# Optimization experiments

Measured on AMD Instinct MI355X. Metric: run time of the kernel, lower is better.

The kernel has to match this reference:

```python
import jax, jax.numpy as jnp
import numpy as np

N_NODES = 50000
N_EDGES = 800000
IN_DIM, HID_DIM, OUT_DIM = 64, 128, 128


def _glorot(key, shape):
    fan_in, fan_out = shape[1], shape[0]
    lim = float(np.sqrt(6.0 / (fan_in + fan_out)))
    return jax.random.uniform(key, shape, jnp.float32, -lim, lim)


def setup_inputs() -> dict:
    key = jax.random.key(0)
    ks = jax.random.split(key, 8)
    x = jax.random.normal(ks[0], (N_NODES, IN_DIM), jnp.float32)
    edge_index = jax.random.randint(ks[1], (2, N_EDGES), 0, N_NODES, jnp.int64)
    return {
        "x": x,
        "edge_index": edge_index,
        # layer 1 (SAGEConv: lin_l acts on aggregated neighbors + bias, lin_r on root)
        "W1_l": _glorot(ks[2], (HID_DIM, IN_DIM)),
        "W1_r": _glorot(ks[3], (HID_DIM, IN_DIM)),
        "b1": jnp.zeros((HID_DIM,), jnp.float32),
        # layer 2
        "W2_l": _glorot(ks[4], (OUT_DIM, HID_DIM)),
        "W2_r": _glorot(ks[5], (OUT_DIM, HID_DIM)),
        "b2": jnp.zeros((OUT_DIM,), jnp.float32),
    }


def _sage_conv(x, src, dst, W_l, W_r, b):
    # mean aggregation of neighbor features: messages flow src -> dst
    msg = x[src]                                           # [E, D]
    agg = jax.ops.segment_sum(msg, dst, num_segments=N_NODES)  # [N, D]
    deg = jax.ops.segment_sum(jnp.ones((msg.shape[0],), x.dtype), dst,
                              num_segments=N_NODES)        # [N]
    mean = agg / jnp.maximum(deg, 1.0)[:, None]            # isolated nodes -> 0
    return mean @ W_l.T + x @ W_r.T + b


def reference(x, edge_index, W1_l, W1_r, b1, W2_l, W2_r, b2):
    src, dst = edge_index[0], edge_index[1]
    h = _sage_conv(x, src, dst, W1_l, W1_r, b1)
    h = jax.nn.relu(h)
    out = _sage_conv(h, src, dst, W2_l, W2_r, b2)
    return out
```

## Files before the change

### kernel.cpp

```cpp
#include <hip/hip_runtime.h>
#include <hip/hip_bf16.h>

constexpr int N  = 50000;
constexpr int E  = 800000;
constexpr int D0 = 64;
constexpr int D1 = 128;
constexpr int CAP = 64;

constexpr int NPART = 8;
constexpr int PSZ   = (N + NPART - 1) / NPART;
constexpr int BPP   = 128;

typedef __attribute__((ext_vector_type(8))) short short8;
typedef __attribute__((ext_vector_type(4))) float f32x4;

__device__ __forceinline__ unsigned short bf16bits(float f) {
    __hip_bfloat16 hb = __float2bfloat16(f);
    return *reinterpret_cast<unsigned short*>(&hb);
}

__device__ __forceinline__ void acc8(float* a, const uint4 r) {
    union { unsigned u; float f; } c;
    c.u = r.x << 16;         a[0] += c.f;
    c.u = r.x & 0xffff0000u; a[1] += c.f;
    c.u = r.y << 16;         a[2] += c.f;
    c.u = r.y & 0xffff0000u; a[3] += c.f;
    c.u = r.z << 16;         a[4] += c.f;
    c.u = r.z & 0xffff0000u; a[5] += c.f;
    c.u = r.w << 16;         a[6] += c.f;
    c.u = r.w & 0xffff0000u; a[7] += c.f;
}

__global__ __launch_bounds__(256)
void k_prep(const float* __restrict__ x, unsigned short* __restrict__ xb,
            const float* __restrict__ W1l, const float* __restrict__ W1r,
            const float* __restrict__ W2l, const float* __restrict__ W2r,
            unsigned short* __restrict__ W1cat, unsigned short* __restrict__ W2cat,
            int* __restrict__ cnt) {
    int i = blockIdx.x * blockDim.x + threadIdx.x;
    if (i < N / 4) ((int4*)cnt)[i] = make_int4(0, 0, 0, 0);
    if (i < 128 * 128) {
        int o = i >> 7, k = i & 127;
        float v = (k < 64) ? W1l[o * 64 + k] : W1r[o * 64 + (k - 64)];
        W1cat[i] = bf16bits(v);
    }
    if (i < 128 * 256) {
        int o = i >> 8, k = i & 255;
        float v = (k < 128) ? W2l[o * 128 + k] : W2r[o * 128 + (k - 128)];
        W2cat[i] = bf16bits(v);
    }
    if (i < N * D0 / 8) {
        const float4 v0 = *(const float4*)&x[(size_t)i * 8];
        const float4 v1 = *(const float4*)&x[(size_t)i * 8 + 4];
        float f[8] = {v0.x, v0.y, v0.z, v0.w, v1.x, v1.y, v1.z, v1.w};
        unsigned short u[8];
        #pragma unroll
        for (int j = 0; j < 8; ++j) u[j] = bf16bits(f[j]);
        *(short8*)&xb[(size_t)i * 8] = *(short8*)u;
    }
}

__global__ __launch_bounds__(256)
void k_bin(const int* __restrict__ src, const int* __restrict__ dst,
           int* __restrict__ cnt, unsigned short* __restrict__ bin) {
    const int p     = blockIdx.x & (NPART - 1);
    const int local = blockIdx.x >> 3;
    const int lo = p * PSZ;
    const int hi = min(N, lo + PSZ);

    for (int i = local * 256 + threadIdx.x; i < E / 4; i += BPP * 256) {
        const int e0 = i * 4;
        int4 d = *(const int4*)&dst[e0];
        int4 s = *(const int4*)&src[e0];
        if (d.x >= lo && d.x < hi) {
            int pos = atomicAdd(&cnt[d.x], 1);
            if (pos < CAP) bin[(size_t)d.x * CAP + pos] = (unsigned short)s.x;
        }
        if (d.y >= lo && d.y < hi) {
            int pos = atomicAdd(&cnt[d.y], 1);
            if (pos < CAP) bin[(size_t)d.y * CAP + pos] = (unsigned short)s.y;
        }
        if (d.z >= lo && d.z < hi) {
            int pos = atomicAdd(&cnt[d.z], 1);
            if (pos < CAP) bin[(size_t)d.z * CAP + pos] = (unsigned short)s.z;
        }
        if (d.w >= lo && d.w < hi) {
            int pos = atomicAdd(&cnt[d.w], 1);
            if (pos < CAP) bin[(size_t)d.w * CAP + pos] = (unsigned short)s.w;
        }
    }
}

template<int DIN>
__global__ __launch_bounds__(256, 8)
void k_gather(const unsigned short* __restrict__ xin,
              const int* __restrict__ cnt,
              const unsigned short* __restrict__ bin,
              unsigned short* __restrict__ mean) {
    constexpr int GRPSZ = DIN / 8;
    constexpr int GPB   = 256 / GRPSZ;
    const int tid      = threadIdx.x;
    const int sub      = tid & (GRPSZ - 1);
    const int gloc     = tid / GRPSZ;
    const int lane     = tid & 63;
    const int lanebase = (lane / GRPSZ) * GRPSZ;
    const int g0   = blockIdx.x * GPB + gloc;
    const int gstr = gridDim.x * GPB;

    for (int n = g0; n < N; n += gstr) {
        const int deg  = cnt[n];
        const int degc = min(deg, CAP);
        const size_t base = (size_t)n * CAP;

        float a[8] = {0.f, 0.f, 0.f, 0.f, 0.f, 0.f, 0.f, 0.f};

        for (int b = 0; b < degc; b += GRPSZ) {
            int nb = (b + sub < degc) ? (int)bin[base + b + sub] : 0;
            const int c = min(GRPSZ, degc - b);
            int j = 0;
            for (; j + 4 <= c; j += 4) {
                int s0 = __shfl(nb, lanebase + j + 0);
                int s1 = __shfl(nb, lanebase + j + 1);
                int s2 = __shfl(nb, lanebase + j + 2);
                int s3 = __shfl(nb, lanebase + j + 3);
                uint4 r0 = *(const uint4*)&xin[(size_t)s0 * DIN + sub * 8];
                uint4 r1 = *(const uint4*)&xin[(size_t)s1 * DIN + sub * 8];
                uint4 r2 = *(const uint4*)&xin[(size_t)s2 * DIN + sub * 8];
                uint4 r3 = *(const uint4*)&xin[(size_t)s3 * DIN + sub * 8];
                acc8(a, r0); acc8(a, r1); acc8(a, r2); acc8(a, r3);
            }
            for (; j < c; ++j) {
                int s = __shfl(nb, lanebase + j);
                uint4 r = *(const uint4*)&xin[(size_t)s * DIN + sub * 8];
                acc8(a, r);
            }
        }

        const float invd = 1.0f / fmaxf((float)deg, 1.0f);
        unsigned short u[8];
        #pragma unroll
        for (int q = 0; q < 8; ++q) u[q] = bf16bits(a[q] * invd);
        *(short8*)&mean[(size_t)n * DIN + sub * 8] = *(short8*)u;
    }
}

template<int DIN, bool RELU, bool OUT_BF16>
__global__ __launch_bounds__(256)
void k_mdense(const unsigned short* __restrict__ mean,
              const unsigned short* __restrict__ xin,
              const unsigned short* __restrict__ Wcat,
              const float* __restrict__ bias,
              void* __restrict__ out,
              int n_nodes) {
    constexpr int K  = 2 * DIN;
    constexpr int KP = K + 8;
    __shared__ unsigned short A[64 * KP];

    const int tid   = threadIdx.x;
    const int nbase = blockIdx.x * 64;

    constexpr int CPR   = K / 8;
    constexpr int TOTAL = 64 * CPR;
    for (int c = tid; c < TOTAL; c += 256) {
        int row  = c / CPR;
        int col8 = (c - row * CPR) * 8;
        int n    = nbase + row;
        short8 v = (short8)0;
        if (n < n_nodes) {
            const unsigned short* srcp = (col8 < DIN)
                ? &mean[(size_t)n * DIN + col8]
                : &xin[(size_t)n * DIN + (col8 - DIN)];
            v = *(const short8*)srcp;
        }
        *(short8*)&A[row * KP + col8] = v;
    }
    __syncthreads();

    const int lane = tid & 63;
    const int wv   = tid >> 6;
    const int l15  = lane & 15;
    const int kseg = lane >> 4;

    f32x4 acc[8];
    #pragma unroll
    for (int ot = 0; ot < 8; ++ot) acc[ot] = (f32x4){0.f, 0.f, 0.f, 0.f};

    #pragma unroll
    for (int kk = 0; kk < K / 32; ++kk) {
        short8 a = *(const short8*)&A[(wv * 16 + l15) * KP + kk * 32 + kseg * 8];
        #pragma unroll
        for (int ot = 0; ot < 8; ++ot) {
            short8 b = *(const short8*)&Wcat[(size_t)(ot * 16 + l15) * K + kk * 32 + kseg * 8];
            acc[ot] = __builtin_amdgcn_mfma_f32_16x16x32_bf16(a, b, acc[ot], 0, 0, 0);
        }
    }

    #pragma unroll
    for (int ot = 0; ot < 8; ++ot) {
        const int o  = ot * 16 + l15;
        const float bv = bias[o];
        #pragma unroll
        for (int i = 0; i < 4; ++i) {
            int n = nbase + wv * 16 + kseg * 4 + i;
            if (n < n_nodes) {
                float v = acc[ot][i] + bv;
                if constexpr (RELU) v = fmaxf(v, 0.0f);
                if constexpr (OUT_BF16) {
                    ((unsigned short*)out)[(size_t)n * 128 + o] = bf16bits(v);
                } else {
                    ((float*)out)[(size_t)n * 128 + o] = v;
                }
            }
        }
    }
}

extern "C" void kernel_launch(void* const* d_in, const int* in_sizes, int n_in,
                              void* d_out, int out_size, void* d_ws, size_t ws_size,
                              hipStream_t stream) {
    const float* x   = (const float*)d_in[0];
    const int*   ei  = (const int*)d_in[1];
    const float* W1l = (const float*)d_in[2];
    const float* W1r = (const float*)d_in[3];
    const float* b1  = (const float*)d_in[4];
    const float* W2l = (const float*)d_in[5];
    const float* W2r = (const float*)d_in[6];
    const float* b2  = (const float*)d_in[7];
    float*       out = (float*)d_out;

    const int* src = ei;
    const int* dst = ei + E;

    char* p = (char*)d_ws;
    auto alloc = [&](size_t bytes) -> char* {
        char* r = p; p += (bytes + 15) & ~(size_t)15; return r;
    };
    int*            cnt   = (int*)alloc(N * sizeof(int));
    unsigned short* bin   = (unsigned short*)alloc((size_t)N * CAP * 2);
    unsigned short* xb    = (unsigned short*)alloc((size_t)N * D0 * 2);
    unsigned short* h     = (unsigned short*)alloc((size_t)N * D1 * 2);
    unsigned short* mean  = (unsigned short*)alloc((size_t)N * D1 * 2);
    unsigned short* W1cat = (unsigned short*)alloc(128 * 128 * 2);
    unsigned short* W2cat = (unsigned short*)alloc(128 * 256 * 2);

    const int nblk_d = (N + 63) / 64;

    k_prep<<<(N * D0 / 8 + 255) / 256, 256, 0, stream>>>(
        x, xb, W1l, W1r, W2l, W2r, W1cat, W2cat, cnt);

    k_bin<<<NPART * BPP, 256, 0, stream>>>(src, dst, cnt, bin);

    k_gather<D0><<<2048, 256, 0, stream>>>(xb, cnt, bin, mean);
    k_mdense<D0, true, true>
        <<<nblk_d, 256, 0, stream>>>(mean, xb, W1cat, b1, h, N);

    k_gather<D1><<<2048, 256, 0, stream>>>(h, cnt, bin, mean);
    k_mdense<D1, false, false>
        <<<nblk_d, 256, 0, stream>>>(mean, h, W2cat, b2, out, N);
}
```

Before: 168.2 us.

## Fuse neighbor mean gather into dense layer kernel via shared memory

Merges the gather kernel into the dense MFMA kernel. Each 64-node block now computes the neighbor means directly into its shared-memory A tile next to the root features, so the mean buffer is no longer written to and read back from global memory, and two launches per layer go away. In exchange, the gather now runs with the dense kernel's grid of about 782 blocks instead of 2048 grid-stride blocks, with fewer nodes in flight per block, so latency hiding and load balance for the irregular gather may suffer.

```diff
diff --git a/kernel.cpp b/kernel.cpp
--- a/kernel.cpp
+++ b/kernel.cpp
@@ -91,67 +91,15 @@
     }
 }
 
-template<int DIN>
-__global__ __launch_bounds__(256, 8)
-void k_gather(const unsigned short* __restrict__ xin,
-              const int* __restrict__ cnt,
-              const unsigned short* __restrict__ bin,
-              unsigned short* __restrict__ mean) {
-    constexpr int GRPSZ = DIN / 8;
-    constexpr int GPB   = 256 / GRPSZ;
-    const int tid      = threadIdx.x;
-    const int sub      = tid & (GRPSZ - 1);
-    const int gloc     = tid / GRPSZ;
-    const int lane     = tid & 63;
-    const int lanebase = (lane / GRPSZ) * GRPSZ;
-    const int g0   = blockIdx.x * GPB + gloc;
-    const int gstr = gridDim.x * GPB;
-
-    for (int n = g0; n < N; n += gstr) {
-        const int deg  = cnt[n];
-        const int degc = min(deg, CAP);
-        const size_t base = (size_t)n * CAP;
-
-        float a[8] = {0.f, 0.f, 0.f, 0.f, 0.f, 0.f, 0.f, 0.f};
-
-        for (int b = 0; b < degc; b += GRPSZ) {
-            int nb = (b + sub < degc) ? (int)bin[base + b + sub] : 0;
-            const int c = min(GRPSZ, degc - b);
-            int j = 0;
-            for (; j + 4 <= c; j += 4) {
-                int s0 = __shfl(nb, lanebase + j + 0);
-                int s1 = __shfl(nb, lanebase + j + 1);
-                int s2 = __shfl(nb, lanebase + j + 2);
-                int s3 = __shfl(nb, lanebase + j + 3);
-                uint4 r0 = *(const uint4*)&xin[(size_t)s0 * DIN + sub * 8];
-                uint4 r1 = *(const uint4*)&xin[(size_t)s1 * DIN + sub * 8];
-                uint4 r2 = *(const uint4*)&xin[(size_t)s2 * DIN + sub * 8];
-                uint4 r3 = *(const uint4*)&xin[(size_t)s3 * DIN + sub * 8];
-                acc8(a, r0); acc8(a, r1); acc8(a, r2); acc8(a, r3);
-            }
-            for (; j < c; ++j) {
-                int s = __shfl(nb, lanebase + j);
-                uint4 r = *(const uint4*)&xin[(size_t)s * DIN + sub * 8];
-                acc8(a, r);
-            }
-        }
-
-        const float invd = 1.0f / fmaxf((float)deg, 1.0f);
-        unsigned short u[8];
-        #pragma unroll
-        for (int q = 0; q < 8; ++q) u[q] = bf16bits(a[q] * invd);
-        *(short8*)&mean[(size_t)n * DIN + sub * 8] = *(short8*)u;
-    }
-}
-
 template<int DIN, bool RELU, bool OUT_BF16>
 __global__ __launch_bounds__(256)
-void k_mdense(const unsigned short* __restrict__ mean,
-              const unsigned short* __restrict__ xin,
-              const unsigned short* __restrict__ Wcat,
-              const float* __restrict__ bias,
-              void* __restrict__ out,
-              int n_nodes) {
+void k_layer(const unsigned short* __restrict__ xin,
+             const int* __restrict__ cnt,
+             const unsigned short* __restrict__ bin,
+             const unsigned short* __restrict__ Wcat,
+             const float* __restrict__ bias,
+             void* __restrict__ out,
+             int n_nodes) {
     constexpr int K  = 2 * DIN;
     constexpr int KP = K + 8;
     __shared__ unsigned short A[64 * KP];
@@ -159,20 +107,65 @@
     const int tid   = threadIdx.x;
     const int nbase = blockIdx.x * 64;
 
-    constexpr int CPR   = K / 8;
-    constexpr int TOTAL = 64 * CPR;
-    for (int c = tid; c < TOTAL; c += 256) {
+    constexpr int CPR = DIN / 8;
+    for (int c = tid; c < 64 * CPR; c += 256) {
         int row  = c / CPR;
         int col8 = (c - row * CPR) * 8;
         int n    = nbase + row;
         short8 v = (short8)0;
-        if (n < n_nodes) {
-            const unsigned short* srcp = (col8 < DIN)
-                ? &mean[(size_t)n * DIN + col8]
-                : &xin[(size_t)n * DIN + (col8 - DIN)];
-            v = *(const short8*)srcp;
-        }
-        *(short8*)&A[row * KP + col8] = v;
+        if (n < n_nodes) v = *(const short8*)&xin[(size_t)n * DIN + col8];
+        *(short8*)&A[row * KP + DIN + col8] = v;
+    }
+
+    {
+        constexpr int GRPSZ = DIN / 8;
+        constexpr int NGRP  = 256 / GRPSZ;
+        constexpr int NPG   = 64 / NGRP;
+        const int sub      = tid & (GRPSZ - 1);
+        const int gloc     = tid / GRPSZ;
+        const int lane     = tid & 63;
+        const int lanebase = (lane / GRPSZ) * GRPSZ;
+
+        #pragma unroll
+        for (int i = 0; i < NPG; ++i) {
+            const int row = gloc * NPG + i;
+            const int n   = nbase + row;
+
+            float a[8] = {0.f, 0.f, 0.f, 0.f, 0.f, 0.f, 0.f, 0.f};
+            int deg = 0;
+            if (n < n_nodes) {
+                deg = cnt[n];
+                const int degc = min(deg, CAP);
+                const size_t base = (size_t)n * CAP;
+                for (int b = 0; b < degc; b += GRPSZ) {
+                    int nb = (b + sub < degc) ? (int)bin[base + b + sub] : 0;
+                    const int c = min(GRPSZ, degc - b);
+                    int j = 0;
+                    for (; j + 4 <= c; j += 4) {
+                        int s0 = __shfl(nb, lanebase + j + 0);
+                        int s1 = __shfl(nb, lanebase + j + 1);
+                        int s2 = __shfl(nb, lanebase + j + 2);
+                        int s3 = __shfl(nb, lanebase + j + 3);
+                        uint4 r0 = *(const uint4*)&xin[(size_t)s0 * DIN + sub * 8];
+                        uint4 r1 = *(const uint4*)&xin[(size_t)s1 * DIN + sub * 8];
+                        uint4 r2 = *(const uint4*)&xin[(size_t)s2 * DIN + sub * 8];
+                        uint4 r3 = *(const uint4*)&xin[(size_t)s3 * DIN + sub * 8];
+                        acc8(a, r0); acc8(a, r1); acc8(a, r2); acc8(a, r3);
+                    }
+                    for (; j < c; ++j) {
+                        int s = __shfl(nb, lanebase + j);
+                        uint4 r = *(const uint4*)&xin[(size_t)s * DIN + sub * 8];
+                        acc8(a, r);
+                    }
+                }
+            }
+
+            const float invd = 1.0f / fmaxf((float)deg, 1.0f);
+            unsigned short u[8];
+            #pragma unroll
+            for (int q = 0; q < 8; ++q) u[q] = bf16bits(a[q] * invd);
+            *(short8*)&A[row * KP + sub * 8] = *(short8*)u;
+        }
     }
     __syncthreads();
 
@@ -239,22 +232,19 @@
     unsigned short* bin   = (unsigned short*)alloc((size_t)N * CAP * 2);
     unsigned short* xb    = (unsigned short*)alloc((size_t)N * D0 * 2);
     unsigned short* h     = (unsigned short*)alloc((size_t)N * D1 * 2);
-    unsigned short* mean  = (unsigned short*)alloc((size_t)N * D1 * 2);
     unsigned short* W1cat = (unsigned short*)alloc(128 * 128 * 2);
     unsigned short* W2cat = (unsigned short*)alloc(128 * 256 * 2);
 
-    const int nblk_d = (N + 63) / 64;
+    const int nblk = (N + 63) / 64;
 
     k_prep<<<(N * D0 / 8 + 255) / 256, 256, 0, stream>>>(
         x, xb, W1l, W1r, W2l, W2r, W1cat, W2cat, cnt);
 
     k_bin<<<NPART * BPP, 256, 0, stream>>>(src, dst, cnt, bin);
 
-    k_gather<D0><<<2048, 256, 0, stream>>>(xb, cnt, bin, mean);
-    k_mdense<D0, true, true>
-        <<<nblk_d, 256, 0, stream>>>(mean, xb, W1cat, b1, h, N);
-
-    k_gather<D1><<<2048, 256, 0, stream>>>(h, cnt, bin, mean);
-    k_mdense<D1, false, false>
-        <<<nblk_d, 256, 0, stream>>>(mean, h, W2cat, b2, out, N);
-}
+    k_layer<D0, true, true>
+        <<<nblk, 256, 0, stream>>>(xb, cnt, bin, W1cat, b1, h, N);
+
+    k_layer<D1, false, false>
+        <<<nblk, 256, 0, stream>>>(h, cnt, bin, W2cat, b2, out, N);
+}
```

Result: faster. 158.6 us (-5.7%).
